# Performance work log

Hardware: AMD Instinct MI355X
Metric: run time of the kernel (lower is better)

## Reference

```python
import jax, jax.numpy as jnp
import numpy as np

B, H, W, C, F = 32, 32, 32, 256, 64
K_NEIGH = 32  # L1 pixel-distance cutoff used for the static mask


def _distance_mask(h, w, k):
    # coords: [hw, 2] of (y, x); L1 pixel distances, normalized by max(h, w)
    ys, xs = jnp.meshgrid(jnp.arange(h), jnp.arange(w), indexing='ij')
    coords = jnp.stack([ys, xs], axis=-1).reshape(-1, 2).astype(jnp.float32)
    diff = jnp.abs(coords[:, None, :] - coords[None, :, :]).sum(-1)  # [hw, hw], == cdist p=1
    dist = diff / float(max(h, w))
    return jnp.where(diff <= k, dist, 0.0)


def setup_inputs() -> dict:
    key = jax.random.key(0)
    ks = jax.random.split(key, 7)
    return {
        'feature_map': jax.random.normal(ks[0], (B, H, W, C), dtype=jnp.float32),
        'emb_W': jax.random.normal(ks[1], (F, C), dtype=jnp.float32) * (1.0 / np.sqrt(C)),
        'emb_b': jax.random.normal(ks[2], (F,), dtype=jnp.float32) * 0.01,
        'attn_W': jax.random.normal(ks[3], (C, C), dtype=jnp.float32) * (1.0 / np.sqrt(C)),
        'attn_b': jax.random.normal(ks[4], (C,), dtype=jnp.float32) * 0.01,
        'thr_W': jax.random.normal(ks[5], (1, C), dtype=jnp.float32) * (1.0 / np.sqrt(C)),
        'thr_b': jax.random.normal(ks[6], (1,), dtype=jnp.float32) * 0.01,
        'layer': 0,
    }


def reference(feature_map, emb_W, emb_b, attn_W, attn_b, thr_W, thr_b, layer):
    b, h, w, c = feature_map.shape
    hw = h * w
    x = feature_map.reshape(b, hw, c)  # row-major (y, x) flatten, matches torch view

    # 1x1 conv -> per-pixel linear: instance embeddings [b, hw, F]
    emb = jnp.einsum('bnc,fc->bnf', x, emb_W) + emb_b

    # squared Euclidean pairwise distances (cdist p=2, then squared)
    sq = jnp.sum(emb * emb, axis=-1)  # [b, hw]
    d2 = jnp.maximum(sq[:, :, None] + sq[:, None, :]
                     - 2.0 * jnp.einsum('bnf,bmf->bnm', emb, emb), 0.0)

    mask = _distance_mask(h, w, K_NEIGH)  # [hw, hw] static buffer
    sim = jax.nn.softmax(jnp.exp(-d2) - (1.0 - mask), axis=-1)  # [b, hw, hw]

    # shortcut = attention_conv(feature_map): [b, hw, c]
    shortcut = jnp.einsum('bnc,dc->bnd', x, attn_W) + attn_b

    # per-pixel learned threshold: [b, hw]
    Tinst = (jnp.einsum('bnc,oc->bno', shortcut, thr_W) + thr_b)[..., 0]

    A = jax.nn.softmax(jnp.maximum(sim - Tinst[:, None, :], 0.0), axis=-1)

    # bmm: out[b, i, c] = sum_j shortcut[b, j, c] * A[b, i, j]
    attn_out = jnp.einsum('bjc,bij->bic', shortcut, A)

    res = (x + attn_out).reshape(b, h, w, c)
    return res
```

## Files before the change

### kernel.cpp

```cpp
#include <hip/hip_runtime.h>
#include <hip/hip_bf16.h>


typedef short bf16x8 __attribute__((ext_vector_type(8)));
typedef float f32x4 __attribute__((ext_vector_type(4)));

__device__ __forceinline__ unsigned short f2bf(float f) {
  unsigned u = __float_as_uint(f);
  u += 0x7fffu + ((u >> 16) & 1u);
  return (unsigned short)(u >> 16);
}
__device__ __forceinline__ float bf2f(unsigned short h) {
  return __uint_as_float(((unsigned)h) << 16);
}
__device__ __forceinline__ unsigned pack2(float a, float b) {
  return (unsigned)f2bf(a) | ((unsigned)f2bf(b) << 16);
}
__device__ __forceinline__ f32x4 mfma16(bf16x8 a, bf16x8 b, f32x4 c) {
  return __builtin_amdgcn_mfma_f32_16x16x32_bf16(a, b, c, 0, 0, 0);
}
__device__ __forceinline__ int iabs(int v) { return v < 0 ? -v : v; }
__device__ __forceinline__ void load_lds16(const void* g, void* l) {
  __builtin_amdgcn_global_load_lds(
      (const __attribute__((address_space(1))) unsigned int*)g,
      (__attribute__((address_space(3))) unsigned int*)l, 16, 0, 0);
}

__global__ __launch_bounds__(256) void k_emb(const float* __restrict__ x,
                                             const float* __restrict__ embW,
                                             const float* __restrict__ embB,
                                             unsigned short* __restrict__ embb,
                                             float* __restrict__ sq) {
  __shared__ unsigned short xs[64][40];
  __shared__ unsigned short ws[64][40];
  __shared__ float sqls[64];
  const int t = threadIdx.x;
  const int Mbase = blockIdx.x * 64;
  const int lane = t & 63, wave = t >> 6;
  const int wm = wave >> 1, wn = wave & 1;
  const int l15 = lane & 15, quad = lane >> 4;

  f32x4 acc[2][2] = {};
  for (int k0 = 0; k0 < 256; k0 += 32) {
    {
      int row = t >> 2, c0 = (t & 3) * 8;
      const float* src = x + (size_t)(Mbase + row) * 256 + k0 + c0;
      float4 a = *(const float4*)src;
      float4 b = *(const float4*)(src + 4);
      uint4 p; p.x = pack2(a.x, a.y); p.y = pack2(a.z, a.w);
      p.z = pack2(b.x, b.y); p.w = pack2(b.z, b.w);
      *(uint4*)&xs[row][c0] = p;
    }
    if (t < 64) {
      const float* wsrc = embW + (size_t)t * 256 + k0;
      for (int s = 0; s < 4; s++) {
        float4 a = *(const float4*)(wsrc + s * 8);
        float4 b = *(const float4*)(wsrc + s * 8 + 4);
        uint4 p; p.x = pack2(a.x, a.y); p.y = pack2(a.z, a.w);
        p.z = pack2(b.x, b.y); p.w = pack2(b.z, b.w);
        *(uint4*)&ws[t][s * 8] = p;
      }
    }
    __syncthreads();
    bf16x8 af[2], bfr[2];
    for (int rt = 0; rt < 2; rt++)
      af[rt] = *(const bf16x8*)&xs[wm * 32 + rt * 16 + l15][quad * 8];
    for (int ct = 0; ct < 2; ct++)
      bfr[ct] = *(const bf16x8*)&ws[wn * 32 + ct * 16 + l15][quad * 8];
    for (int rt = 0; rt < 2; rt++)
      for (int ct = 0; ct < 2; ct++)
        acc[rt][ct] = mfma16(af[rt], bfr[ct], acc[rt][ct]);
    __syncthreads();
  }

  if (t < 64) sqls[t] = 0.f;
  __syncthreads();
  float sp[2][4] = {};
  for (int rt = 0; rt < 2; rt++)
    for (int ct = 0; ct < 2; ct++) {
      int f = wn * 32 + ct * 16 + l15;
      float bias = embB[f];
      for (int r = 0; r < 4; r++) {
        float v = acc[rt][ct][r] + bias;
        unsigned short hb = f2bf(v);
        int rowl = wm * 32 + rt * 16 + quad * 4 + r;
        embb[(size_t)(Mbase + rowl) * 64 + f] = hb;
        float vf = bf2f(hb);
        sp[rt][r] += vf * vf;
      }
    }
  for (int m = 8; m >= 1; m >>= 1)
    for (int rt = 0; rt < 2; rt++)
      for (int r = 0; r < 4; r++)
        sp[rt][r] += __shfl_xor(sp[rt][r], m);
  if (l15 == 0)
    for (int rt = 0; rt < 2; rt++)
      for (int r = 0; r < 4; r++)
        atomicAdd(&sqls[wm * 32 + rt * 16 + quad * 4 + r], sp[rt][r]);
  __syncthreads();
  if (t < 64) sq[Mbase + t] = sqls[t];
}

__global__ __launch_bounds__(256) void k_shortcut(const float* __restrict__ x,
                                                  const float* __restrict__ attnW,
                                                  const float* __restrict__ attnB,
                                                  const float* __restrict__ thrW,
                                                  const float* __restrict__ thrB,
                                                  unsigned short* __restrict__ scT,
                                                  float* __restrict__ Tout) {
  __shared__ unsigned short xs[64][40];
  __shared__ unsigned short ws[256][40];
  __shared__ unsigned short St[256][72];
  const int t = threadIdx.x;
  const int Mbase = blockIdx.x * 64;
  const int lane = t & 63, wave = t >> 6;
  const int wm = wave >> 1, wn = wave & 1;
  const int l15 = lane & 15, quad = lane >> 4;

  f32x4 acc[2][8] = {};
  for (int k0 = 0; k0 < 256; k0 += 32) {
    {
      int row = t >> 2, c0 = (t & 3) * 8;
      const float* src = x + (size_t)(Mbase + row) * 256 + k0 + c0;
      float4 a = *(const float4*)src;
      float4 b = *(const float4*)(src + 4);
      uint4 p; p.x = pack2(a.x, a.y); p.y = pack2(a.z, a.w);
      p.z = pack2(b.x, b.y); p.w = pack2(b.z, b.w);
      *(uint4*)&xs[row][c0] = p;
    }
    {
      const float* wsrc = attnW + (size_t)t * 256 + k0;
      for (int s = 0; s < 4; s++) {
        float4 a = *(const float4*)(wsrc + s * 8);
        float4 b = *(const float4*)(wsrc + s * 8 + 4);
        uint4 p; p.x = pack2(a.x, a.y); p.y = pack2(a.z, a.w);
        p.z = pack2(b.x, b.y); p.w = pack2(b.z, b.w);
        *(uint4*)&ws[t][s * 8] = p;
      }
    }
    __syncthreads();
    bf16x8 af[2];
    for (int rt = 0; rt < 2; rt++)
      af[rt] = *(const bf16x8*)&xs[wm * 32 + rt * 16 + l15][quad * 8];
    for (int nt = 0; nt < 8; nt++) {
      bf16x8 bfr = *(const bf16x8*)&ws[wn * 128 + nt * 16 + l15][quad * 8];
      for (int rt = 0; rt < 2; rt++)
        acc[rt][nt] = mfma16(af[rt], bfr, acc[rt][nt]);
    }
    __syncthreads();
  }

  for (int rt = 0; rt < 2; rt++)
    for (int nt = 0; nt < 8; nt++) {
      int c = wn * 128 + nt * 16 + l15;
      float bias = attnB[c];
      for (int r = 0; r < 4; r++) {
        float v = acc[rt][nt][r] + bias;
        int j = wm * 32 + rt * 16 + quad * 4 + r;
        St[c][j] = f2bf(v);
      }
    }
  __syncthreads();
  const int b = Mbase >> 10, jbase = Mbase & 1023;
  {
    unsigned short* dst = scT + ((size_t)b * 256 + t) * 1024 + jbase;
    for (int s = 0; s < 8; s++)
      *(uint4*)(dst + s * 8) = *(const uint4*)&St[t][s * 8];
  }
  {
    float tp = 0.f;
    int j = t >> 2, cs = (t & 3) * 64;
    for (int c = 0; c < 64; c++)
      tp += bf2f(St[cs + c][j]) * thrW[cs + c];
    tp += __shfl_xor(tp, 1);
    tp += __shfl_xor(tp, 2);
    if ((t & 3) == 0) Tout[Mbase + j] = tp + thrB[0];
  }
}

__global__ __launch_bounds__(256) void k_scores(const unsigned short* __restrict__ embb,
                                                const float* __restrict__ sq,
                                                const float* __restrict__ T,
                                                unsigned short* __restrict__ U,
                                                float* __restrict__ Z) {
  __shared__ float rbuf[64];
  const int t = threadIdx.x, lane = t & 63, wave = t >> 6;
  const int bid = blockIdx.x;
  const int b = bid >> 4, rb = (bid & 15) * 64;
  const int l15 = lane & 15, quad = lane >> 4;
  const unsigned short* eb = embb + (size_t)b * 1024 * 64;
  const int rowA = rb + wave * 16 + l15;
  bf16x8 a0 = *(const bf16x8*)(eb + (size_t)rowA * 64 + quad * 8);
  bf16x8 a1 = *(const bf16x8*)(eb + (size_t)rowA * 64 + 32 + quad * 8);
  const int rowC = rb + wave * 16 + quad * 4;
  float sqi[4]; int yi[4], xi[4];
  for (int r = 0; r < 4; r++) {
    sqi[r] = sq[b * 1024 + rowC + r];
    yi[r] = (rowC + r) >> 5; xi[r] = (rowC + r) & 31;
  }
  float rp[4] = {0.f, 0.f, 0.f, 0.f};
  for (int j0 = 0; j0 < 1024; j0 += 16) {
    const int jr = j0 + l15;
    bf16x8 b0 = *(const bf16x8*)(eb + (size_t)jr * 64 + quad * 8);
    bf16x8 b1 = *(const bf16x8*)(eb + (size_t)jr * 64 + 32 + quad * 8);
    f32x4 g = {0.f, 0.f, 0.f, 0.f};
    g = mfma16(a0, b0, g);
    g = mfma16(a1, b1, g);
    float sqj = sq[b * 1024 + jr];
    int yj = jr >> 5, xj = jr & 31;
    for (int r = 0; r < 4; r++) {
      float d2 = fmaxf(sqi[r] + sqj - 2.f * g[r], 0.f);
      int diff = iabs(yi[r] - yj) + iabs(xi[r] - xj);
      float m = (diff <= 32) ? (float)diff * (1.f / 32.f) : 0.f;
      float s = __expf(-d2) - 1.f + m;
      unsigned short h = f2bf(__expf(s));
      U[((size_t)(b * 1024 + rowC + r)) * 1024 + jr] = h;
      rp[r] += bf2f(h);
    }
  }
  for (int m = 8; m >= 1; m >>= 1)
    for (int r = 0; r < 4; r++)
      rp[r] += __shfl_xor(rp[r], m);
  if (l15 == 0)
    for (int r = 0; r < 4; r++)
      rbuf[wave * 16 + quad * 4 + r] = rp[r];
  __syncthreads();

  const int prow = lane >> 2, q = lane & 3;
  const float invR = 1.f / rbuf[wave * 16 + prow];
  unsigned short* ur = U + ((size_t)(b * 1024 + rb + wave * 16 + prow)) * 1024;
  const float* Tb = T + b * 1024;
  float z = 0.f;
  for (int jc = 0; jc < 1024; jc += 32) {
    int j = jc + q * 8;
    union { uint4 v; unsigned short s[8]; } ev;
    ev.v = *(const uint4*)(ur + j);
    float4 t0 = *(const float4*)(Tb + j);
    float4 t1 = *(const float4*)(Tb + j + 4);
    float tf[8] = {t0.x, t0.y, t0.z, t0.w, t1.x, t1.y, t1.z, t1.w};
    union { uint4 v; unsigned short s[8]; } uo;
    for (int k = 0; k < 8; k++) {
      float u = __expf(fmaxf(fmaf(bf2f(ev.s[k]), invR, -tf[k]), 0.f));
      unsigned short h = f2bf(u);
      uo.s[k] = h;
      z += bf2f(h);
    }
    *(uint4*)(ur + j) = uo.v;
  }
  z += __shfl_xor(z, 1);
  z += __shfl_xor(z, 2);
  if (q == 0) Z[b * 1024 + rb + wave * 16 + prow] = z;
}

__global__ __launch_bounds__(256) void k_out(const unsigned short* __restrict__ U,
                                             const float* __restrict__ Z,
                                             const unsigned short* __restrict__ scT,
                                             const float* __restrict__ x,
                                             float* __restrict__ out) {
  __shared__ unsigned short Ab[128 * 32];
  __shared__ unsigned short Bb[128 * 32];
  const int t = threadIdx.x, lane = t & 63, wave = t >> 6;
  const int wm = wave >> 1, wn = wave & 1;
  const int l15 = lane & 15, quad = lane >> 4;
  const int x8 = blockIdx.x & 7, s = blockIdx.x >> 3;
  const int b = x8 * 4 + (s >> 4), tile = s & 15;
  const int rb = (tile >> 1) * 128, cb = (tile & 1) * 128;

  const unsigned short* Ubase = U + (size_t)b * 1024 * 1024 + (size_t)rb * 1024;
  const unsigned short* Sbase = scT + (size_t)b * 256 * 1024 + (size_t)cb * 1024;

  int c0 = wave * 64 + lane;
  int c1 = c0 + 256;
  const int r0 = c0 >> 2, o0 = (c0 & 3) * 8;
  const int r1 = c1 >> 2, o1 = (c1 & 3) * 8;

  f32x4 acc[4][4] = {};
  for (int j0 = 0; j0 < 1024; j0 += 32) {
    load_lds16(Ubase + (size_t)r0 * 1024 + j0 + o0, Ab + c0 * 8);
    load_lds16(Ubase + (size_t)r1 * 1024 + j0 + o1, Ab + c1 * 8);
    load_lds16(Sbase + (size_t)r0 * 1024 + j0 + o0, Bb + c0 * 8);
    load_lds16(Sbase + (size_t)r1 * 1024 + j0 + o1, Bb + c1 * 8);
    __syncthreads();
    bf16x8 af[4], bf[4];
    for (int i = 0; i < 4; i++)
      af[i] = *(const bf16x8*)&Ab[(wm * 64 + i * 16 + l15) * 32 + quad * 8];
    for (int i = 0; i < 4; i++)
      bf[i] = *(const bf16x8*)&Bb[(wn * 64 + i * 16 + l15) * 32 + quad * 8];
    for (int i = 0; i < 4; i++)
      for (int j = 0; j < 4; j++)
        acc[i][j] = mfma16(af[i], bf[j], acc[i][j]);
    __syncthreads();
  }

  const int colb = cb + wn * 64;
  for (int i = 0; i < 4; i++) {
    int rowb = rb + wm * 64 + i * 16 + quad * 4;
    float iz[4];
    for (int r = 0; r < 4; r++) iz[r] = 1.f / Z[b * 1024 + rowb + r];
    for (int j = 0; j < 4; j++) {
      int c = colb + j * 16 + l15;
      for (int r = 0; r < 4; r++) {
        size_t idx = ((size_t)(b * 1024 + rowb + r)) * 256 + c;
        out[idx] = x[idx] + acc[i][j][r] * iz[r];
      }
    }
  }
}

extern "C" void kernel_launch(void* const* d_in, const int* in_sizes, int n_in,
                              void* d_out, int out_size, void* d_ws, size_t ws_size,
                              hipStream_t stream) {
  const float* x     = (const float*)d_in[0];
  const float* embW  = (const float*)d_in[1];
  const float* embB  = (const float*)d_in[2];
  const float* attnW = (const float*)d_in[3];
  const float* attnB = (const float*)d_in[4];
  const float* thrW  = (const float*)d_in[5];
  const float* thrB  = (const float*)d_in[6];
  float* out = (float*)d_out;

  char* ws = (char*)d_ws;
  unsigned short* embb = (unsigned short*)(ws);
  unsigned short* scT  = (unsigned short*)(ws + (4ull << 20));
  unsigned short* U    = (unsigned short*)(ws + (20ull << 20));
  float* sq = (float*)(ws + (84ull << 20));
  float* T  = (float*)(ws + (84ull << 20) + (128ull << 10));
  float* Z  = (float*)(ws + (84ull << 20) + (256ull << 10));

  k_emb<<<512, 256, 0, stream>>>(x, embW, embB, embb, sq);
  k_shortcut<<<512, 256, 0, stream>>>(x, attnW, attnB, thrW, thrB, scT, T);
  k_scores<<<512, 256, 0, stream>>>(embb, sq, T, U, Z);
  k_out<<<512, 256, 0, stream>>>(U, Z, scT, x, out);
}
```

Before: 219.2 us.

## Stage first-pass softmax scores in LDS instead of round-tripping through global U

k_scores now handles 16 rows per block, with each wave covering a quarter of the columns. The first-softmax numerators are written to an LDS tile and the row sums are combined with shared atomics, so the second pass reads from LDS instead of rereading global memory. This removes one full write and one full read of the large bf16 U matrix and raises the grid from 512 to 2048 blocks. In exchange each block uses about 33KB of LDS and needs an extra barrier, which may lower occupancy.

```diff
diff --git a/kernel.cpp b/kernel.cpp
--- a/kernel.cpp
+++ b/kernel.cpp
@@ -183,23 +183,28 @@
                                                 const float* __restrict__ T,
                                                 unsigned short* __restrict__ U,
                                                 float* __restrict__ Z) {
-  __shared__ float rbuf[64];
+  __shared__ unsigned short E_lds[16 * 1040];
+  __shared__ float rbuf[16];
   const int t = threadIdx.x, lane = t & 63, wave = t >> 6;
-  const int bid = blockIdx.x;
-  const int b = bid >> 4, rb = (bid & 15) * 64;
+  const int b = blockIdx.x >> 6, rb = (blockIdx.x & 63) * 16;
   const int l15 = lane & 15, quad = lane >> 4;
   const unsigned short* eb = embb + (size_t)b * 1024 * 64;
-  const int rowA = rb + wave * 16 + l15;
+
+  if (t < 16) rbuf[t] = 0.f;
+
+  const int rowA = rb + l15;
   bf16x8 a0 = *(const bf16x8*)(eb + (size_t)rowA * 64 + quad * 8);
   bf16x8 a1 = *(const bf16x8*)(eb + (size_t)rowA * 64 + 32 + quad * 8);
-  const int rowC = rb + wave * 16 + quad * 4;
+  const int rloc = quad * 4;
   float sqi[4]; int yi[4], xi[4];
   for (int r = 0; r < 4; r++) {
-    sqi[r] = sq[b * 1024 + rowC + r];
-    yi[r] = (rowC + r) >> 5; xi[r] = (rowC + r) & 31;
-  }
+    int rowg = rb + rloc + r;
+    sqi[r] = sq[b * 1024 + rowg];
+    yi[r] = rowg >> 5; xi[r] = rowg & 31;
+  }
+  const int jq = wave * 256;
   float rp[4] = {0.f, 0.f, 0.f, 0.f};
-  for (int j0 = 0; j0 < 1024; j0 += 16) {
+  for (int j0 = jq; j0 < jq + 256; j0 += 16) {
     const int jr = j0 + l15;
     bf16x8 b0 = *(const bf16x8*)(eb + (size_t)jr * 64 + quad * 8);
     bf16x8 b1 = *(const bf16x8*)(eb + (size_t)jr * 64 + 32 + quad * 8);
@@ -214,27 +219,28 @@
       float m = (diff <= 32) ? (float)diff * (1.f / 32.f) : 0.f;
       float s = __expf(-d2) - 1.f + m;
       unsigned short h = f2bf(__expf(s));
-      U[((size_t)(b * 1024 + rowC + r)) * 1024 + jr] = h;
+      E_lds[(rloc + r) * 1040 + jr] = h;
       rp[r] += bf2f(h);
     }
   }
   for (int m = 8; m >= 1; m >>= 1)
     for (int r = 0; r < 4; r++)
       rp[r] += __shfl_xor(rp[r], m);
+  __syncthreads();
   if (l15 == 0)
     for (int r = 0; r < 4; r++)
-      rbuf[wave * 16 + quad * 4 + r] = rp[r];
-  __syncthreads();
-
-  const int prow = lane >> 2, q = lane & 3;
-  const float invR = 1.f / rbuf[wave * 16 + prow];
-  unsigned short* ur = U + ((size_t)(b * 1024 + rb + wave * 16 + prow)) * 1024;
+      atomicAdd(&rbuf[rloc + r], rp[r]);
+  __syncthreads();
+
+  const int prow = t >> 4, seg = t & 15;
+  const float invR = 1.f / rbuf[prow];
   const float* Tb = T + b * 1024;
+  unsigned short* ur = U + ((size_t)(b * 1024 + rb + prow)) * 1024;
   float z = 0.f;
-  for (int jc = 0; jc < 1024; jc += 32) {
-    int j = jc + q * 8;
-    union { uint4 v; unsigned short s[8]; } ev;
-    ev.v = *(const uint4*)(ur + j);
+  for (int c = 0; c < 8; c++) {
+    int j = c * 128 + seg * 8;
+    union { bf16x8 v; unsigned short s[8]; } ev;
+    ev.v = *(const bf16x8*)&E_lds[prow * 1040 + j];
     float4 t0 = *(const float4*)(Tb + j);
     float4 t1 = *(const float4*)(Tb + j + 4);
     float tf[8] = {t0.x, t0.y, t0.z, t0.w, t1.x, t1.y, t1.z, t1.w};
@@ -249,7 +255,9 @@
   }
   z += __shfl_xor(z, 1);
   z += __shfl_xor(z, 2);
-  if (q == 0) Z[b * 1024 + rb + wave * 16 + prow] = z;
+  z += __shfl_xor(z, 4);
+  z += __shfl_xor(z, 8);
+  if (seg == 0) Z[b * 1024 + rb + prow] = z;
 }
 
 __global__ __launch_bounds__(256) void k_out(const unsigned short* __restrict__ U,
@@ -329,6 +337,6 @@
 
   k_emb<<<512, 256, 0, stream>>>(x, embW, embB, embb, sq);
   k_shortcut<<<512, 256, 0, stream>>>(x, attnW, attnB, thrW, thrB, scT, T);
-  k_scores<<<512, 256, 0, stream>>>(embb, sq, T, U, Z);
+  k_scores<<<2048, 256, 0, stream>>>(embb, sq, T, U, Z);
   k_out<<<512, 256, 0, stream>>>(U, Z, scT, x, out);
 }
```

Result: faster. 208.2 us (-5.0%).
